# Optimization experiments

Hardware: AMD Instinct MI355X
Metric: run time of the kernel (lower is better)

The kernel has to match this reference:

```python
import jax, jax.numpy as jnp
import numpy as np

N = 50000        # nodes
E = 800000       # edges
F_IN = 64
HID = [128, 256, 256]
G = 512          # graphs in batch
C = 6            # classes
EPS = 1e-5


def setup_inputs() -> dict:
    key = jax.random.key(0)
    ks = jax.random.split(key, 32)
    inp = {}
    inp['x'] = jax.random.normal(ks[0], (N, F_IN), dtype=jnp.float32)
    inp['edge_index'] = jax.random.randint(ks[1], (2, E), 0, N, dtype=jnp.int64)
    inp['batch'] = jnp.sort(jax.random.randint(ks[2], (N,), 0, G, dtype=jnp.int64))
    dims = [F_IN] + HID
    i = 3
    for l in range(3):
        d_in, d_out = dims[l], dims[l + 1]
        inp[f'W{l+1}'] = jax.random.normal(ks[i], (d_in, d_out), dtype=jnp.float32) * (1.0 / np.sqrt(d_in)); i += 1
        inp[f'b{l+1}'] = jnp.zeros((d_out,), dtype=jnp.float32)
        inp[f'g{l+1}'] = jnp.ones((d_out,), dtype=jnp.float32)
        inp[f'be{l+1}'] = jnp.zeros((d_out,), dtype=jnp.float32)
        inp[f'm{l+1}'] = jax.random.normal(ks[i], (d_out,), dtype=jnp.float32) * 0.1; i += 1
        inp[f'v{l+1}'] = jax.random.uniform(ks[i], (d_out,), dtype=jnp.float32, minval=0.5, maxval=1.5); i += 1
    mlp_dims = [(2 * HID[-1], 256), (256, 128), (128, C)]
    for l, (d_in, d_out) in enumerate(mlp_dims):
        inp[f'Wm{l+1}'] = jax.random.normal(ks[i], (d_in, d_out), dtype=jnp.float32) * (1.0 / np.sqrt(d_in)); i += 1
        inp[f'bm{l+1}'] = jnp.zeros((d_out,), dtype=jnp.float32)
    return inp


def _forward(x, edge_index, batch,
             W1, b1, g1, be1, m1, v1,
             W2, b2, g2, be2, m2, v2,
             W3, b3, g3, be3, m3, v3,
             Wm1, bm1, Wm2, bm2, Wm3, bm3):
    src, dst = edge_index[0], edge_index[1]
    loops = jnp.arange(N, dtype=src.dtype)
    src_sl = jnp.concatenate([src, loops])   # self-loops, as in PyG GCNConv
    dst_sl = jnp.concatenate([dst, loops])
    deg = jax.ops.segment_sum(jnp.ones_like(src_sl, dtype=x.dtype), dst_sl, num_segments=N)
    dis = jnp.where(deg > 0, jax.lax.rsqrt(deg), 0.0)
    norm = dis[src_sl] * dis[dst_sl]          # [E+N]

    def gcn(h, W, b):
        h = h @ W                              # transform first (PyG order)
        msg = h[src_sl] * norm[:, None]        # gather + scale
        return jax.ops.segment_sum(msg, dst_sl, num_segments=N) + b

    def bn_relu(h, g, be, m, v):
        return jax.nn.relu((h - m) * jax.lax.rsqrt(v + EPS) * g + be)

    h = bn_relu(gcn(x, W1, b1), g1, be1, m1, v1)
    h = bn_relu(gcn(h, W2, b2), g2, be2, m2, v2)
    h = bn_relu(gcn(h, W3, b3), g3, be3, m3, v3)

    counts = jax.ops.segment_sum(jnp.ones((N,), dtype=h.dtype), batch, num_segments=G)
    x_mean = jax.ops.segment_sum(h, batch, num_segments=G) / jnp.maximum(counts, 1.0)[:, None]
    x_max = jax.ops.segment_max(h, batch, num_segments=G)
    x_max = jnp.where(counts[:, None] > 0, x_max, 0.0)
    z = jnp.concatenate([x_mean, x_max], axis=1)   # [G, 512]

    z = jax.nn.gelu(z @ Wm1 + bm1, approximate=False)
    z = jax.nn.gelu(z @ Wm2 + bm2, approximate=False)
    return z @ Wm3 + bm3                            # [G, C]


def reference(x, edge_index, batch,
              W1, b1, g1, be1, m1, v1,
              W2, b2, g2, be2, m2, v2,
              W3, b3, g3, be3, m3, v3,
              Wm1, bm1, Wm2, bm2, Wm3, bm3):
    return _forward(x, edge_index, batch,
                    W1, b1, g1, be1, m1, v1,
                    W2, b2, g2, be2, m2, v2,
                    W3, b3, g3, be3, m3, v3,
                    Wm1, bm1, Wm2, bm2, Wm3, bm3)
```

## Files before the change

kernel.cpp:

```cpp
#include <hip/hip_runtime.h>
#include <hip/hip_bf16.h>
#include <hip/hip_fp16.h>

typedef __hip_bfloat16 bf16;
typedef unsigned short u16;
typedef short bfrag __attribute__((ext_vector_type(8)));
typedef float f32x4 __attribute__((ext_vector_type(4)));
typedef unsigned u32x2 __attribute__((ext_vector_type(2)));

#define NGRAPH 512
#define BN_EPS 1e-5f
#define NBUCK 64

__device__ __forceinline__ float b2f(bf16 x) { return __bfloat162float(x); }
__device__ __forceinline__ float bf_lo(unsigned u) { return __uint_as_float(u << 16); }
__device__ __forceinline__ float bf_hi(unsigned u) { return __uint_as_float(u & 0xffff0000u); }
__device__ __forceinline__ u16 f2u(float v) {
    bf16 t = __float2bfloat16(v);
    u16 r; __builtin_memcpy(&r, &t, 2); return r;
}

__device__ __forceinline__ float load_f(const void* p, int i, int isbf16) {
    if (isbf16) {
        unsigned short u = ((const unsigned short*)p)[i];
        return __uint_as_float(((unsigned int)u) << 16);
    }
    return ((const float*)p)[i];
}

__global__ void detect_dtype(const void* __restrict__ x, int* __restrict__ flag) {
    int lane = threadIdx.x & 63;
    unsigned short u = ((const unsigned short*)x)[2 * lane];
    float f = __uint_as_float(((unsigned int)u) << 16);
    int crazy = (!(fabsf(f) <= 1024.0f)) ? 1 : 0;
    unsigned long long m = __ballot(crazy);
    if (threadIdx.x == 0) *flag = (m == 0ULL) ? 1 : 0;
}

__global__ void cvt_bf_s(const void* __restrict__ in, u16* __restrict__ out,
                         int n, int npad, const int* __restrict__ flag) {
    int i = blockIdx.x * blockDim.x + threadIdx.x;
    if (i >= n * 64) return;
    int node = i >> 6, f = i & 63;
    out[((size_t)(f >> 5) * npad + node) * 32 + (f & 31)] = f2u(load_f(in, i, *flag));
}

__global__ void repack_w(const void* __restrict__ W, u16* __restrict__ out,
                         int Kd, int Nd, const int* __restrict__ flag) {
    int t = blockIdx.x * blockDim.x + threadIdx.x;
    if (t >= Kd * Nd) return;
    int isbf = *flag;
    int j = t & 7;
    int lane = (t >> 3) & 63;
    int tile = t >> 9;
    int NT = Nd / 16;
    int nt = tile % NT, kt = tile / NT;
    int k = kt * 32 + (lane >> 4) * 8 + j;
    int nn = nt * 16 + (lane & 15);
    out[t] = f2u(load_f(W, k * Nd + nn, isbf));
}

__device__ __forceinline__ void fold_one(const void* b, const void* g, const void* be,
                                         const void* m, const void* v,
                                         float* S, float* T, int f, int isbf) {
    float bb = load_f(b, f, isbf), gg = load_f(g, f, isbf);
    float bee = load_f(be, f, isbf), mm = load_f(m, f, isbf);
    float vv = load_f(v, f, isbf);
    float s = gg * rsqrtf(vv + BN_EPS);
    S[f] = s;
    T[f] = (bb - mm) * s + bee;
}

__global__ void fold_bn_all(
    const void* b1, const void* g1, const void* be1, const void* m1, const void* v1,
    const void* b2, const void* g2, const void* be2, const void* m2, const void* v2,
    const void* b3, const void* g3, const void* be3, const void* m3, const void* v3,
    float* S1, float* T1, float* S2, float* T2, float* S3, float* T3,
    const int* __restrict__ flag) {
    int t = blockIdx.x * blockDim.x + threadIdx.x;
    int isbf = *flag;
    if (t < 128) fold_one(b1, g1, be1, m1, v1, S1, T1, t, isbf);
    else if (t < 384) fold_one(b2, g2, be2, m2, v2, S2, T2, t - 128, isbf);
    else if (t < 640) fold_one(b3, g3, be3, m3, v3, S3, T3, t - 384, isbf);
}

__global__ void init_csr(int* __restrict__ deg, int* __restrict__ total,
                         int* __restrict__ bcnt, int n) {
    int i = blockIdx.x * blockDim.x + threadIdx.x;
    if (i < n) deg[i] = 0;
    if (i < NBUCK) bcnt[i] = 0;
    if (i == 0) *total = 0;
}

__global__ void count_deg_i(const int* __restrict__ dst, int* __restrict__ deg, int e) {
    int i = blockIdx.x * blockDim.x + threadIdx.x;
    if (i < e) atomicAdd(&deg[dst[i]], 1);
}

__global__ void reserve_rows(const int* __restrict__ deg, int* __restrict__ row_start,
                             int* __restrict__ cursor, float* __restrict__ dis,
                             unsigned* __restrict__ csrw,
                             int* __restrict__ total, int* __restrict__ bcnt, int n) {
    __shared__ int lh[NBUCK];
    int tid = threadIdx.x;
    if (tid < NBUCK) lh[tid] = 0;
    __syncthreads();
    int i = blockIdx.x * blockDim.x + tid;
    if (i < n) {
        int d = deg[i];
        int dpad = (d + 7) & ~7;
        int s = atomicAdd(total, dpad);
        row_start[i] = s;
        cursor[i] = s;
        dis[i] = rsqrtf((float)(d + 1));
        atomicAdd(&lh[min(d, NBUCK - 1)], 1);
        unsigned val = (unsigned)(i & 0xffff);
        for (int k = d; k < dpad; k++) csrw[s + k] = val;
    }
    __syncthreads();
    if (tid < NBUCK) {
        int c = lh[tid];
        if (c) atomicAdd(&bcnt[tid], c);
    }
}

__global__ void bucket_prefix(const int* __restrict__ bcnt, int* __restrict__ bcur) {
    if (threadIdx.x == 0 && blockIdx.x == 0) {
        int acc = 0;
        for (int i = 0; i < NBUCK; i++) { bcur[i] = acc; acc += bcnt[i]; }
    }
}

__global__ void bucket_scatter(const int* __restrict__ deg, const int* __restrict__ rowst,
                               int* __restrict__ bcur, uint4* __restrict__ ninfo, int n) {
    __shared__ int lh[NBUCK];
    __shared__ int lbase[NBUCK];
    int tid = threadIdx.x;
    if (tid < NBUCK) lh[tid] = 0;
    __syncthreads();
    int i = blockIdx.x * blockDim.x + tid;
    int b = 0, lr = 0;
    if (i < n) {
        b = min(deg[i], NBUCK - 1);
        lr = atomicAdd(&lh[b], 1);
    }
    __syncthreads();
    if (tid < NBUCK) {
        int c = lh[tid];
        lbase[tid] = c ? atomicAdd(&bcur[tid], c) : 0;
    }
    __syncthreads();
    if (i < n) ninfo[lbase[b] + lr] = make_uint4(i, rowst[i], deg[i], 0);
}

__global__ void scatter_edges(const int* __restrict__ src, const int* __restrict__ dst,
                              const float* __restrict__ dis, int* __restrict__ cursor,
                              unsigned* __restrict__ csrw, int e) {
    int i = blockIdx.x * blockDim.x + threadIdx.x;
    if (i >= e) return;
    int s = src[i], dt = dst[i];
    int pos = atomicAdd(&cursor[dt], 1);
    float nw = dis[s] * dis[dt];
    unsigned short h = __half_as_ushort(__float2half(nw));
    csrw[pos] = (unsigned)(s & 0xffff) | ((unsigned)h << 16);
}

template <int NSLICE>
__global__ __launch_bounds__(256) void csr_agg_s5(
    const uint4* __restrict__ ninfo, const unsigned* __restrict__ csrw,
    const u16* __restrict__ hs, u16* __restrict__ AG, int n, int npad) {
    constexpr int F = NSLICE * 32;
    int slice = blockIdx.x % NSLICE;
    int nb = blockIdx.x / NSLICE;
    int lane = threadIdx.x & 63;
    int wv = threadIdx.x >> 6;
    int sub = lane >> 3, ls = lane & 7;
    int oidx = nb * 32 + wv * 8 + sub;
    if (oidx >= n) return;
    uint4 nf = ninfo[oidx];
    int node = (int)nf.x;
    int start = (int)nf.y;
    int d = (int)nf.z;
    int dpad = (d + 7) & ~7;
    float dd = 1.0f / (float)(d + 1);
    const u16* __restrict__ base = hs + (size_t)slice * npad * 32;

    float a0, a1, a2, a3;
    {
        uint2 u = *(const uint2*)(base + (size_t)node * 32 + ls * 4);
        a0 = bf_lo(u.x) * dd; a1 = bf_hi(u.x) * dd;
        a2 = bf_lo(u.y) * dd; a3 = bf_hi(u.y) * dd;
    }

    const unsigned* __restrict__ ep = csrw + start;
    unsigned mc[8];
    if (dpad) {
#pragma unroll
        for (int j = 0; j < 8; j++) mc[j] = ep[j];
    }
    for (int k = 0; k < dpad; k += 8) {
        unsigned mn[8];
        if (k + 8 < dpad) {
#pragma unroll
            for (int j = 0; j < 8; j++) mn[j] = ep[k + 8 + j];
        }
        float w[8];
        uint2 q[8];
#pragma unroll
        for (int j = 0; j < 8; j++) {
            int s = (int)(mc[j] & 0xffffu);
            w[j] = __half2float(__ushort_as_half((unsigned short)(mc[j] >> 16)));
            q[j] = *(const uint2*)(base + (size_t)s * 32 + ls * 4);
        }
#pragma unroll
        for (int j = 0; j < 8; j++) {
            a0 += w[j] * bf_lo(q[j].x); a1 += w[j] * bf_hi(q[j].x);
            a2 += w[j] * bf_lo(q[j].y); a3 += w[j] * bf_hi(q[j].y);
        }
#pragma unroll
        for (int j = 0; j < 8; j++) mc[j] = mn[j];
    }
    u32x2 o;
    o.x = (unsigned)f2u(a0) | ((unsigned)f2u(a1) << 16);
    o.y = (unsigned)f2u(a2) | ((unsigned)f2u(a3) << 16);
    __builtin_nontemporal_store(o, (u32x2*)(AG + (size_t)node * F + slice * 32 + ls * 4));
}

template <int K, int N, int NSUB, int NSLICE_OUT>
__global__ __launch_bounds__(256) void mfma_gemm_rb(
    const u16* __restrict__ A, const u16* __restrict__ Wrep,
    const float* __restrict__ S, const float* __restrict__ T,
    u16* __restrict__ C, int M, int npad) {
    constexpr int KP = K + 8;
    constexpr int NT = N / 16;
    constexpr int KT = K / 32;
    constexpr int NSPLIT = NT / NSUB;
    __shared__ u16 Alds[64 * KP];
    const int mt = blockIdx.x / NSPLIT;
    const int ns = blockIdx.x - mt * NSPLIT;
    const int m0 = mt * 64;
    const int tid = threadIdx.x;
    const int lane = tid & 63;
    const int wv = tid >> 6;

    bfrag breg[KT * NSUB];
#pragma unroll
    for (int kt = 0; kt < KT; kt++)
#pragma unroll
        for (int j = 0; j < NSUB; j++)
            breg[kt * NSUB + j] = *(const bfrag*)(Wrep +
                ((size_t)(kt * NT + ns * NSUB + j) * 64 + lane) * 8);

    for (int c = tid; c < 64 * (K / 8); c += 256) {
        int r = c / (K / 8), kc = c % (K / 8);
        uint4 v = *(const uint4*)(A + (size_t)(m0 + r) * K + kc * 8);
        *(uint4*)(&Alds[r * KP + kc * 8]) = v;
    }
    __syncthreads();

    const int mrow = lane & 15;
    const int kb = lane >> 4;
    f32x4 acc[NSUB];
#pragma unroll
    for (int j = 0; j < NSUB; j++) acc[j] = (f32x4){0.f, 0.f, 0.f, 0.f};
#pragma unroll
    for (int kt = 0; kt < KT; kt++) {
        bfrag a = *(const bfrag*)(&Alds[(wv * 16 + mrow) * KP + kt * 32 + kb * 8]);
#pragma unroll
        for (int j = 0; j < NSUB; j++)
            acc[j] = __builtin_amdgcn_mfma_f32_16x16x32_bf16(a, breg[kt * NSUB + j], acc[j], 0, 0, 0);
    }
#pragma unroll
    for (int j = 0; j < NSUB; j++) {
        int f = (ns * NSUB + j) * 16 + mrow;
        float s = S[f];
        float t = T[f];
#pragma unroll
        for (int r = 0; r < 4; r++) {
            int row = m0 + wv * 16 + kb * 4 + r;
            if (row < M) {
                u16 val = f2u(fmaxf(acc[j][r] * s + t, 0.0f));
                if (NSLICE_OUT > 0)
                    C[((size_t)(f >> 5) * npad + row) * 32 + (f & 31)] = val;
                else
                    C[(size_t)row * N + f] = val;
            }
        }
    }
}

__global__ void init_pool(float* __restrict__ psum, float* __restrict__ pmax,
                          int* __restrict__ pcnt) {
    int i = blockIdx.x * blockDim.x + threadIdx.x;
    if (i < NGRAPH * 256) { psum[i] = 0.f; pmax[i] = 0.f; }
    if (i < NGRAPH) pcnt[i] = 0;
}

#define POOL_NC 64
__global__ __launch_bounds__(256) void pool_seg(
    const u16* __restrict__ h, const int* __restrict__ batch,
    float* __restrict__ psum, float* __restrict__ pmax,
    int* __restrict__ pcnt, int n) {
    int wid = (int)(((size_t)blockIdx.x * blockDim.x + threadIdx.x) >> 6);
    int lane = threadIdx.x & 63;
    int n0 = wid * POOL_NC;
    if (n0 >= n) return;
    int n1 = min(n0 + POOL_NC, n);

    float sum[4] = {0.f, 0.f, 0.f, 0.f};
    float mx[4] = {0.f, 0.f, 0.f, 0.f};
    int cnt = 0;
    int gcur = batch[n0];

    uint2 u_next = *(const uint2*)(h + (size_t)n0 * 256 + lane * 4);
    int g_next = gcur;

    for (int node = n0; node < n1; node++) {
        uint2 u = u_next;
        int g = g_next;
        if (node + 1 < n1) {
            u_next = *(const uint2*)(h + (size_t)(node + 1) * 256 + lane * 4);
            g_next = batch[node + 1];
        }
        if (g != gcur) {
#pragma unroll
            for (int c = 0; c < 4; c++) {
                atomicAdd(&psum[gcur * 256 + lane * 4 + c], sum[c]);
                atomicMax((int*)&pmax[gcur * 256 + lane * 4 + c], __float_as_int(mx[c]));
                sum[c] = 0.f; mx[c] = 0.f;
            }
            if (lane == 0) atomicAdd(&pcnt[gcur], cnt);
            cnt = 0;
            gcur = g;
        }
        float v0 = bf_lo(u.x), v1 = bf_hi(u.x), v2 = bf_lo(u.y), v3 = bf_hi(u.y);
        sum[0] += v0; sum[1] += v1; sum[2] += v2; sum[3] += v3;
        mx[0] = fmaxf(mx[0], v0); mx[1] = fmaxf(mx[1], v1);
        mx[2] = fmaxf(mx[2], v2); mx[3] = fmaxf(mx[3], v3);
        cnt++;
    }
#pragma unroll
    for (int c = 0; c < 4; c++) {
        atomicAdd(&psum[gcur * 256 + lane * 4 + c], sum[c]);
        atomicMax((int*)&pmax[gcur * 256 + lane * 4 + c], __float_as_int(mx[c]));
    }
    if (lane == 0) atomicAdd(&pcnt[gcur], cnt);
}

__global__ void build_z(const float* __restrict__ psum, const float* __restrict__ pmax,
                        const int* __restrict__ pcnt, float* __restrict__ z) {
    int i = blockIdx.x * blockDim.x + threadIdx.x;
    if (i >= NGRAPH * 256) return;
    int g = i >> 8, f = i & 255;
    float c = (float)max(pcnt[g], 1);
    z[g * 512 + f] = psum[i] / c;
    z[g * 512 + 256 + f] = pmax[i];
}

template <int K, int NOUT, bool GELU>
__global__ void mlp_gemm(const float* __restrict__ A, const void* __restrict__ W,
                         const void* __restrict__ bias, float* __restrict__ C,
                         const int* __restrict__ flag) {
    __shared__ float a[K];
    int row = blockIdx.x;
    for (int idx = threadIdx.x; idx < K; idx += blockDim.x) a[idx] = A[row * K + idx];
    __syncthreads();
    int col = threadIdx.x;
    if (col < NOUT) {
        int isbf = *flag;
        float acc = load_f(bias, col, isbf);
        if (isbf) {
            const bf16* w = (const bf16*)W;
            for (int k = 0; k < K; k++) acc += a[k] * b2f(w[k * NOUT + col]);
        } else {
            const float* w = (const float*)W;
            for (int k = 0; k < K; k++) acc += a[k] * w[k * NOUT + col];
        }
        if (GELU) acc = 0.5f * acc * (1.0f + erff(acc * 0.70710678118654752f));
        C[row * NOUT + col] = acc;
    }
}

__global__ void write_out(const float* __restrict__ in, void* __restrict__ out,
                          int n, const int* __restrict__ flag) {
    int i = blockIdx.x * blockDim.x + threadIdx.x;
    if (i >= n) return;
    if (*flag) ((bf16*)out)[i] = __float2bfloat16(in[i]);
    else       ((float*)out)[i] = in[i];
}

extern "C" void kernel_launch(void* const* d_in, const int* in_sizes, int n_in,
                              void* d_out, int out_size, void* d_ws, size_t ws_size,
                              hipStream_t stream) {
    const void* x     = d_in[0];
    const int*  ei    = (const int*)d_in[1];
    const int*  batch = (const int*)d_in[2];
    const void *W1 = d_in[3],  *b1 = d_in[4],  *g1 = d_in[5],  *be1 = d_in[6],  *m1 = d_in[7],  *v1 = d_in[8];
    const void *W2 = d_in[9],  *b2 = d_in[10], *g2 = d_in[11], *be2 = d_in[12], *m2 = d_in[13], *v2 = d_in[14];
    const void *W3 = d_in[15], *b3 = d_in[16], *g3 = d_in[17], *be3 = d_in[18], *m3 = d_in[19], *v3 = d_in[20];
    const void *Wm1 = d_in[21], *bm1 = d_in[22];
    const void *Wm2 = d_in[23], *bm2 = d_in[24];
    const void *Wm3 = d_in[25], *bm3 = d_in[26];

    const int n = in_sizes[0] / 64;
    const int E = in_sizes[1] / 2;
    const int* src = ei;
    const int* dst = ei + E;
    const int npad = (n + 63 + 64) & ~63;

    size_t off = 0;
    auto carve = [&](size_t bytes) {
        void* p = (char*)d_ws + off;
        off += (bytes + 255) & ~(size_t)255;
        return p;
    };
    int*      flag  = (int*)carve(4);
    int*      total = (int*)carve(4);
    int*      bcnt  = (int*)carve(NBUCK * 4);
    int*      bcur  = (int*)carve(NBUCK * 4);
    float*    dis   = (float*)carve((size_t)n * 4);
    int*      deg_i = (int*)carve((size_t)n * 4);
    int*      rowst = (int*)carve((size_t)n * 4);
    int*      curs  = (int*)carve((size_t)n * 4);
    uint4*    ninfo = (uint4*)carve((size_t)n * 16);
    unsigned* csrw  = (unsigned*)carve(((size_t)E + 8 * (size_t)n) * 4);
    u16*      xs    = (u16*)carve((size_t)npad * 64 * 2);
    u16*      Hs    = (u16*)carve((size_t)npad * 256 * 2);
    u16*      AG    = (u16*)carve((size_t)npad * 256 * 2);
    u16*      H     = (u16*)carve((size_t)npad * 256 * 2);
    u16*      W1r   = (u16*)carve((size_t)64 * 128 * 2);
    u16*      W2r   = (u16*)carve((size_t)128 * 256 * 2);
    u16*      W3r   = (u16*)carve((size_t)256 * 256 * 2);
    float* S1 = (float*)carve(128 * 4); float* T1 = (float*)carve(128 * 4);
    float* S2 = (float*)carve(256 * 4); float* T2 = (float*)carve(256 * 4);
    float* S3 = (float*)carve(256 * 4); float* T3 = (float*)carve(256 * 4);
    float* psum = (float*)carve((size_t)NGRAPH * 256 * 4);
    float* pmax = (float*)carve((size_t)NGRAPH * 256 * 4);
    int*   pcnt = (int*)carve((size_t)NGRAPH * 4);
    float* z    = (float*)carve((size_t)NGRAPH * 512 * 4);
    float* z1   = (float*)carve((size_t)NGRAPH * 256 * 4);
    float* z2   = (float*)carve((size_t)NGRAPH * 128 * 4);
    float* z3   = (float*)carve((size_t)NGRAPH * 8 * 4);
    (void)ws_size; (void)n_in;

    const int BT = 256;

    detect_dtype<<<1, 64, 0, stream>>>(x, flag);
    cvt_bf_s<<<(n * 64 + BT - 1) / BT, BT, 0, stream>>>(x, xs, n, npad, flag);
    repack_w<<<(64 * 128 + BT - 1) / BT, BT, 0, stream>>>(W1, W1r, 64, 128, flag);
    repack_w<<<(128 * 256 + BT - 1) / BT, BT, 0, stream>>>(W2, W2r, 128, 256, flag);
    repack_w<<<(256 * 256 + BT - 1) / BT, BT, 0, stream>>>(W3, W3r, 256, 256, flag);
    fold_bn_all<<<3, 256, 0, stream>>>(b1, g1, be1, m1, v1, b2, g2, be2, m2, v2,
                                       b3, g3, be3, m3, v3, S1, T1, S2, T2, S3, T3, flag);

    init_csr<<<(n + BT - 1) / BT, BT, 0, stream>>>(deg_i, total, bcnt, n);
    count_deg_i<<<(E + BT - 1) / BT, BT, 0, stream>>>(dst, deg_i, E);
    reserve_rows<<<(n + BT - 1) / BT, BT, 0, stream>>>(deg_i, rowst, curs, dis, csrw, total, bcnt, n);
    bucket_prefix<<<1, 64, 0, stream>>>(bcnt, bcur);
    bucket_scatter<<<(n + BT - 1) / BT, BT, 0, stream>>>(deg_i, rowst, bcur, ninfo, n);
    scatter_edges<<<(E + BT - 1) / BT, BT, 0, stream>>>(src, dst, dis, curs, csrw, E);

    const int gblocks = (n + 63) / 64;
    const int nb32 = (n + 31) / 32;

    csr_agg_s5<2><<<2 * nb32, 256, 0, stream>>>(ninfo, csrw, xs, AG, n, npad);
    mfma_gemm_rb<64, 128, 8, 4><<<gblocks, 256, 0, stream>>>(AG, W1r, S1, T1, Hs, n, npad);

    csr_agg_s5<4><<<4 * nb32, 256, 0, stream>>>(ninfo, csrw, Hs, AG, n, npad);
    mfma_gemm_rb<128, 256, 4, 8><<<gblocks * 4, 256, 0, stream>>>(AG, W2r, S2, T2, Hs, n, npad);

    csr_agg_s5<8><<<8 * nb32, 256, 0, stream>>>(ninfo, csrw, Hs, AG, n, npad);
    mfma_gemm_rb<256, 256, 4, 0><<<gblocks * 4, 256, 0, stream>>>(AG, W3r, S3, T3, H, n, npad);

    init_pool<<<(NGRAPH * 256 + BT - 1) / BT, BT, 0, stream>>>(psum, pmax, pcnt);
    const int pool_waves = (n + POOL_NC - 1) / POOL_NC;
    pool_seg<<<(pool_waves * 64 + BT - 1) / BT, BT, 0, stream>>>(H, batch, psum, pmax, pcnt, n);
    build_z<<<(NGRAPH * 256 + BT - 1) / BT, BT, 0, stream>>>(psum, pmax, pcnt, z);

    mlp_gemm<512, 256, true><<<NGRAPH, 256, 0, stream>>>(z, Wm1, bm1, z1, flag);
    mlp_gemm<256, 128, true><<<NGRAPH, 256, 0, stream>>>(z1, Wm2, bm2, z2, flag);
    mlp_gemm<128, 6, false><<<NGRAPH, 128, 0, stream>>>(z2, Wm3, bm3, z3, flag);
    write_out<<<(NGRAPH * 6 + BT - 1) / BT, BT, 0, stream>>>(z3, d_out, NGRAPH * 6, flag);
}
```

Measured before the change: 461.3 us.

## Make node GEMMs persistent with register-prefetched A tiles across row tiles

Replaces the one-tile-per-block GEMM with a persistent kernel of 512 blocks. Each block keeps its weight fragments in registers and loops over row tiles, prefetching the next A tile into registers while running MFMAs on the current one. This avoids reloading weights for every 64-row tile and hides global load latency behind compute. In exchange it adds register pressure, two barriers per tile, and fewer blocks than SMs-times-occupancy might want.

After: 520.8 us. 1.13x slower.

```diff
diff --git a/kernel.cpp b/kernel.cpp
--- a/kernel.cpp
+++ b/kernel.cpp
@@ -226,22 +226,23 @@
     __builtin_nontemporal_store(o, (u32x2*)(AG + (size_t)node * F + slice * 32 + ls * 4));
 }
 
-template <int K, int N, int NSUB, int NSLICE_OUT>
-__global__ __launch_bounds__(256) void mfma_gemm_rb(
+template <int K, int N, int NSUB, int NSLICE_OUT, int NBLK>
+__global__ __launch_bounds__(256) void mfma_gemm_p(
     const u16* __restrict__ A, const u16* __restrict__ Wrep,
     const float* __restrict__ S, const float* __restrict__ T,
-    u16* __restrict__ C, int M, int npad) {
+    u16* __restrict__ C, int M, int npad, int ntiles) {
     constexpr int KP = K + 8;
     constexpr int NT = N / 16;
     constexpr int KT = K / 32;
-    constexpr int NSPLIT = NT / NSUB;
+    constexpr int NU4 = (64 * (K / 8)) / 256;
     __shared__ u16 Alds[64 * KP];
-    const int mt = blockIdx.x / NSPLIT;
-    const int ns = blockIdx.x - mt * NSPLIT;
-    const int m0 = mt * 64;
+    const int ns = blockIdx.x / NBLK;
+    const int b = blockIdx.x % NBLK;
     const int tid = threadIdx.x;
     const int lane = tid & 63;
     const int wv = tid >> 6;
+    const int mrow = lane & 15;
+    const int kb = lane >> 4;
 
     bfrag breg[KT * NSUB];
 #pragma unroll
@@ -251,41 +252,61 @@
             breg[kt * NSUB + j] = *(const bfrag*)(Wrep +
                 ((size_t)(kt * NT + ns * NSUB + j) * 64 + lane) * 8);
 
-    for (int c = tid; c < 64 * (K / 8); c += 256) {
-        int r = c / (K / 8), kc = c % (K / 8);
-        uint4 v = *(const uint4*)(A + (size_t)(m0 + r) * K + kc * 8);
-        *(uint4*)(&Alds[r * KP + kc * 8]) = v;
-    }
-    __syncthreads();
-
-    const int mrow = lane & 15;
-    const int kb = lane >> 4;
-    f32x4 acc[NSUB];
-#pragma unroll
-    for (int j = 0; j < NSUB; j++) acc[j] = (f32x4){0.f, 0.f, 0.f, 0.f};
-#pragma unroll
-    for (int kt = 0; kt < KT; kt++) {
-        bfrag a = *(const bfrag*)(&Alds[(wv * 16 + mrow) * KP + kt * 32 + kb * 8]);
-#pragma unroll
-        for (int j = 0; j < NSUB; j++)
-            acc[j] = __builtin_amdgcn_mfma_f32_16x16x32_bf16(a, breg[kt * NSUB + j], acc[j], 0, 0, 0);
-    }
-#pragma unroll
-    for (int j = 0; j < NSUB; j++) {
-        int f = (ns * NSUB + j) * 16 + mrow;
-        float s = S[f];
-        float t = T[f];
-#pragma unroll
-        for (int r = 0; r < 4; r++) {
-            int row = m0 + wv * 16 + kb * 4 + r;
-            if (row < M) {
-                u16 val = f2u(fmaxf(acc[j][r] * s + t, 0.0f));
-                if (NSLICE_OUT > 0)
-                    C[((size_t)(f >> 5) * npad + row) * 32 + (f & 31)] = val;
-                else
-                    C[(size_t)row * N + f] = val;
+    int rr[NU4], kk[NU4];
+#pragma unroll
+    for (int i = 0; i < NU4; i++) {
+        int c = tid + i * 256;
+        rr[i] = c / (K / 8);
+        kk[i] = (c % (K / 8)) * 8;
+    }
+
+    uint4 pre[NU4];
+    int mt = b;
+    if (mt < ntiles) {
+#pragma unroll
+        for (int i = 0; i < NU4; i++)
+            pre[i] = *(const uint4*)(A + (size_t)(mt * 64 + rr[i]) * K + kk[i]);
+    }
+    for (; mt < ntiles; mt += NBLK) {
+#pragma unroll
+        for (int i = 0; i < NU4; i++)
+            *(uint4*)(&Alds[rr[i] * KP + kk[i]]) = pre[i];
+        __syncthreads();
+        int mtn = mt + NBLK;
+        if (mtn < ntiles) {
+#pragma unroll
+            for (int i = 0; i < NU4; i++)
+                pre[i] = *(const uint4*)(A + (size_t)(mtn * 64 + rr[i]) * K + kk[i]);
+        }
+        f32x4 acc[NSUB];
+#pragma unroll
+        for (int j = 0; j < NSUB; j++) acc[j] = (f32x4){0.f, 0.f, 0.f, 0.f};
+#pragma unroll
+        for (int kt = 0; kt < KT; kt++) {
+            bfrag a = *(const bfrag*)(&Alds[(wv * 16 + mrow) * KP + kt * 32 + kb * 8]);
+#pragma unroll
+            for (int j = 0; j < NSUB; j++)
+                acc[j] = __builtin_amdgcn_mfma_f32_16x16x32_bf16(a, breg[kt * NSUB + j], acc[j], 0, 0, 0);
+        }
+        const int m0 = mt * 64;
+#pragma unroll
+        for (int j = 0; j < NSUB; j++) {
+            int f = (ns * NSUB + j) * 16 + mrow;
+            float s = S[f];
+            float t = T[f];
+#pragma unroll
+            for (int r = 0; r < 4; r++) {
+                int row = m0 + wv * 16 + kb * 4 + r;
+                if (row < M) {
+                    u16 val = f2u(fmaxf(acc[j][r] * s + t, 0.0f));
+                    if (NSLICE_OUT > 0)
+                        C[((size_t)(f >> 5) * npad + row) * 32 + (f & 31)] = val;
+                    else
+                        C[(size_t)row * N + f] = val;
+                }
             }
         }
+        __syncthreads();
     }
 }
 
@@ -407,6 +428,7 @@
     const int* src = ei;
     const int* dst = ei + E;
     const int npad = (n + 63 + 64) & ~63;
+    const int ntiles = (n + 63) / 64;
 
     size_t off = 0;
     auto carve = [&](size_t bytes) {
@@ -460,17 +482,16 @@
     bucket_scatter<<<(n + BT - 1) / BT, BT, 0, stream>>>(deg_i, rowst, bcur, ninfo, n);
     scatter_edges<<<(E + BT - 1) / BT, BT, 0, stream>>>(src, dst, dis, curs, csrw, E);
 
-    const int gblocks = (n + 63) / 64;
     const int nb32 = (n + 31) / 32;
 
     csr_agg_s5<2><<<2 * nb32, 256, 0, stream>>>(ninfo, csrw, xs, AG, n, npad);
-    mfma_gemm_rb<64, 128, 8, 4><<<gblocks, 256, 0, stream>>>(AG, W1r, S1, T1, Hs, n, npad);
+    mfma_gemm_p<64, 128, 8, 4, 512><<<512, 256, 0, stream>>>(AG, W1r, S1, T1, Hs, n, npad, ntiles);
 
     csr_agg_s5<4><<<4 * nb32, 256, 0, stream>>>(ninfo, csrw, Hs, AG, n, npad);
-    mfma_gemm_rb<128, 256, 4, 8><<<gblocks * 4, 256, 0, stream>>>(AG, W2r, S2, T2, Hs, n, npad);
+    mfma_gemm_p<128, 256, 4, 8, 128><<<512, 256, 0, stream>>>(AG, W2r, S2, T2, Hs, n, npad, ntiles);
 
     csr_agg_s5<8><<<8 * nb32, 256, 0, stream>>>(ninfo, csrw, Hs, AG, n, npad);
-    mfma_gemm_rb<256, 256, 4, 0><<<gblocks * 4, 256, 0, stream>>>(AG, W3r, S3, T3, H, n, npad);
+    mfma_gemm_p<256, 256, 4, 0, 128><<<512, 256, 0, stream>>>(AG, W3r, S3, T3, H, n, npad, ntiles);
 
     init_pool<<<(NGRAPH * 256 + BT - 1) / BT, BT, 0, stream>>>(psum, pmax, pcnt);
     const int pool_waves = (n + POOL_NC - 1) / POOL_NC;
```

## Load GEMM A fragments directly to registers and remap blocks across N splits

Applied to the files above, without the earlier changes.

The MFMA GEMM no longer stages the 64-row A tile through LDS with a block barrier. Each wave now loads its own A fragments straight from global memory into registers. Block indices are remapped so eight consecutive blocks share one N-split, which is meant to improve L2 reuse of the weight slice and the A rows. NSUB is reduced for layers 1 and 3, giving more blocks with fewer registers each. The cost is strided, non-coalesced 16-byte global loads per lane instead of cooperative coalesced loads, and A is re-read more often across the extra N-splits.

Result: no change. 458.7 us (-0.6%).

```diff
diff --git a/kernel.cpp b/kernel.cpp
--- a/kernel.cpp
+++ b/kernel.cpp
@@ -227,21 +227,23 @@
 }
 
 template <int K, int N, int NSUB, int NSLICE_OUT>
-__global__ __launch_bounds__(256) void mfma_gemm_rb(
+__global__ __launch_bounds__(256) void mfma_gemm_dg(
     const u16* __restrict__ A, const u16* __restrict__ Wrep,
     const float* __restrict__ S, const float* __restrict__ T,
-    u16* __restrict__ C, int M, int npad) {
-    constexpr int KP = K + 8;
+    u16* __restrict__ C, int M, int npad, int ntiles) {
     constexpr int NT = N / 16;
     constexpr int KT = K / 32;
     constexpr int NSPLIT = NT / NSUB;
-    __shared__ u16 Alds[64 * KP];
-    const int mt = blockIdx.x / NSPLIT;
-    const int ns = blockIdx.x - mt * NSPLIT;
-    const int m0 = mt * 64;
+    int bid = blockIdx.x;
+    int g = bid >> 3;
+    int ns = g % NSPLIT;
+    int mt = (bid & 7) + 8 * (g / NSPLIT);
+    if (mt >= ntiles) return;
     const int tid = threadIdx.x;
     const int lane = tid & 63;
     const int wv = tid >> 6;
+    const int mrow = lane & 15;
+    const int kb = lane >> 4;
 
     bfrag breg[KT * NSUB];
 #pragma unroll
@@ -251,25 +253,22 @@
             breg[kt * NSUB + j] = *(const bfrag*)(Wrep +
                 ((size_t)(kt * NT + ns * NSUB + j) * 64 + lane) * 8);
 
-    for (int c = tid; c < 64 * (K / 8); c += 256) {
-        int r = c / (K / 8), kc = c % (K / 8);
-        uint4 v = *(const uint4*)(A + (size_t)(m0 + r) * K + kc * 8);
-        *(uint4*)(&Alds[r * KP + kc * 8]) = v;
-    }
-    __syncthreads();
-
-    const int mrow = lane & 15;
-    const int kb = lane >> 4;
+    const u16* __restrict__ arow = A + (size_t)(mt * 64 + wv * 16 + mrow) * K + kb * 8;
+    bfrag areg[KT];
+#pragma unroll
+    for (int kt = 0; kt < KT; kt++)
+        areg[kt] = *(const bfrag*)(arow + kt * 32);
+
     f32x4 acc[NSUB];
 #pragma unroll
     for (int j = 0; j < NSUB; j++) acc[j] = (f32x4){0.f, 0.f, 0.f, 0.f};
 #pragma unroll
-    for (int kt = 0; kt < KT; kt++) {
-        bfrag a = *(const bfrag*)(&Alds[(wv * 16 + mrow) * KP + kt * 32 + kb * 8]);
+    for (int kt = 0; kt < KT; kt++)
 #pragma unroll
         for (int j = 0; j < NSUB; j++)
-            acc[j] = __builtin_amdgcn_mfma_f32_16x16x32_bf16(a, breg[kt * NSUB + j], acc[j], 0, 0, 0);
-    }
+            acc[j] = __builtin_amdgcn_mfma_f32_16x16x32_bf16(areg[kt], breg[kt * NSUB + j], acc[j], 0, 0, 0);
+
+    const int m0 = mt * 64;
 #pragma unroll
     for (int j = 0; j < NSUB; j++) {
         int f = (ns * NSUB + j) * 16 + mrow;
@@ -407,6 +406,8 @@
     const int* src = ei;
     const int* dst = ei + E;
     const int npad = (n + 63 + 64) & ~63;
+    const int ntiles = (n + 63) / 64;
+    const int ntp8 = (ntiles + 7) & ~7;
 
     size_t off = 0;
     auto carve = [&](size_t bytes) {
@@ -460,17 +461,16 @@
     bucket_scatter<<<(n + BT - 1) / BT, BT, 0, stream>>>(deg_i, rowst, bcur, ninfo, n);
     scatter_edges<<<(E + BT - 1) / BT, BT, 0, stream>>>(src, dst, dis, curs, csrw, E);
 
-    const int gblocks = (n + 63) / 64;
     const int nb32 = (n + 31) / 32;
 
     csr_agg_s5<2><<<2 * nb32, 256, 0, stream>>>(ninfo, csrw, xs, AG, n, npad);
-    mfma_gemm_rb<64, 128, 8, 4><<<gblocks, 256, 0, stream>>>(AG, W1r, S1, T1, Hs, n, npad);
+    mfma_gemm_dg<64, 128, 4, 4><<<2 * ntp8, 256, 0, stream>>>(AG, W1r, S1, T1, Hs, n, npad, ntiles);
 
     csr_agg_s5<4><<<4 * nb32, 256, 0, stream>>>(ninfo, csrw, Hs, AG, n, npad);
-    mfma_gemm_rb<128, 256, 4, 8><<<gblocks * 4, 256, 0, stream>>>(AG, W2r, S2, T2, Hs, n, npad);
+    mfma_gemm_dg<128, 256, 4, 8><<<4 * ntp8, 256, 0, stream>>>(AG, W2r, S2, T2, Hs, n, npad, ntiles);
 
     csr_agg_s5<8><<<8 * nb32, 256, 0, stream>>>(ninfo, csrw, Hs, AG, n, npad);
-    mfma_gemm_rb<256, 256, 4, 0><<<gblocks * 4, 256, 0, stream>>>(AG, W3r, S3, T3, H, n, npad);
+    mfma_gemm_dg<256, 256, 2, 0><<<8 * ntp8, 256, 0, stream>>>(AG, W3r, S3, T3, H, n, npad, ntiles);
 
     init_pool<<<(NGRAPH * 256 + BT - 1) / BT, BT, 0, stream>>>(psum, pmax, pcnt);
     const int pool_waves = (n + POOL_NC - 1) / POOL_NC;
```
